# Optimization experiments

Hardware: AMD Instinct MI355X
Metric: run time of the kernel (lower is better)

Reference implementation:

```python
import jax, jax.numpy as jnp
import numpy as np

B, S, D, H, DK, F, K = 8, 1024, 512, 8, 64, 2048, 31
EPS = 1e-5


def _ln(x, g, b):
    m = jnp.mean(x, -1, keepdims=True)
    v = jnp.mean((x - m) ** 2, -1, keepdims=True)
    return (x - m) * jax.lax.rsqrt(v + EPS) * g + b


def _ff(x, w1, b1, w2, b2):
    return jnp.maximum(x @ w1 + b1, 0.0) @ w2 + b2


def setup_inputs() -> dict:
    key = jax.random.key(0)
    ks = jax.random.split(key, 16)
    w = lambda k, shape: jax.random.normal(k, shape, dtype=jnp.float32) * 0.02
    inp = {"x": jax.random.normal(ks[0], (B, S, D), dtype=jnp.float32)}
    for name in ["norm1", "norm2", "norm3", "norm4", "conv_ln"]:
        inp[name + "_g"] = jnp.ones((D,), jnp.float32)
        inp[name + "_b"] = jnp.zeros((D,), jnp.float32)
    # feed-forward 1 and 2
    inp["ff1_w1"] = w(ks[1], (D, F)); inp["ff1_b1"] = jnp.zeros((F,), jnp.float32)
    inp["ff1_w2"] = w(ks[2], (F, D)); inp["ff1_b2"] = jnp.zeros((D,), jnp.float32)
    inp["ff2_w1"] = w(ks[3], (D, F)); inp["ff2_b1"] = jnp.zeros((F,), jnp.float32)
    inp["ff2_w2"] = w(ks[4], (F, D)); inp["ff2_b2"] = jnp.zeros((D,), jnp.float32)
    # attention projections ([in, out] layout)
    inp["wq"] = w(ks[5], (D, D)); inp["bq"] = jnp.zeros((D,), jnp.float32)
    inp["wk"] = w(ks[6], (D, D)); inp["bk"] = jnp.zeros((D,), jnp.float32)
    inp["wv"] = w(ks[7], (D, D)); inp["bv"] = jnp.zeros((D,), jnp.float32)
    inp["wo"] = w(ks[8], (D, D)); inp["bo"] = jnp.zeros((D,), jnp.float32)
    # convolution module
    inp["pw1_w"] = w(ks[9], (D, 2 * D)); inp["pw1_b"] = jnp.zeros((2 * D,), jnp.float32)
    inp["dw_w"] = w(ks[10], (D, 1, K)); inp["dw_b"] = jnp.zeros((D,), jnp.float32)
    inp["bn_g"] = jnp.ones((D,), jnp.float32); inp["bn_b"] = jnp.zeros((D,), jnp.float32)
    inp["bn_mean"] = jnp.zeros((D,), jnp.float32); inp["bn_var"] = jnp.ones((D,), jnp.float32)
    inp["pw2_w"] = w(ks[11], (D, D)); inp["pw2_b"] = jnp.zeros((D,), jnp.float32)
    return inp


def _forward(x, norm1_g, norm1_b, norm2_g, norm2_b, norm3_g, norm3_b, norm4_g, norm4_b,
             ff1_w1, ff1_b1, ff1_w2, ff1_b2, wq, bq, wk, bk, wv, bv, wo, bo,
             conv_ln_g, conv_ln_b, pw1_w, pw1_b, dw_w, dw_b,
             bn_g, bn_b, bn_mean, bn_var, pw2_w, pw2_b,
             ff2_w1, ff2_b1, ff2_w2, ff2_b2):
    b, s, _ = x.shape
    # half-step FF1
    x = x + 0.5 * _ff(_ln(x, norm1_g, norm1_b), ff1_w1, ff1_b1, ff1_w2, ff1_b2)
    # multi-head self-attention (pre-norm)
    h = _ln(x, norm2_g, norm2_b)
    q = (h @ wq + bq).reshape(b, s, H, DK)
    k = (h @ wk + bk).reshape(b, s, H, DK)
    v = (h @ wv + bv).reshape(b, s, H, DK)
    scores = jnp.einsum("bqhd,bkhd->bhqk", q, k) / jnp.sqrt(jnp.asarray(DK, x.dtype))
    attn = jax.nn.softmax(scores, axis=-1)
    o = jnp.einsum("bhqk,bkhd->bqhd", attn, v).reshape(b, s, D)
    x = x + (o @ wo + bo)
    # convolution module (pre-norm)
    h = _ln(x, norm3_g, norm3_b)
    h = _ln(h, conv_ln_g, conv_ln_b)
    h = h @ pw1_w + pw1_b                                 # [B,S,2D] pointwise conv1
    h = h[..., :D] * jax.nn.sigmoid(h[..., D:])           # GLU over channels
    h = h.transpose(0, 2, 1)                              # [B,D,S]
    h = jax.lax.conv_general_dilated(
        h, dw_w, window_strides=(1,), padding=((K // 2, K // 2),),
        feature_group_count=D, dimension_numbers=("NCH", "OIH", "NCH")) + dw_b[:, None]
    h = (h - bn_mean[:, None]) * jax.lax.rsqrt(bn_var + EPS)[:, None] * bn_g[:, None] + bn_b[:, None]
    h = h * jax.nn.sigmoid(h)                             # SiLU
    h = jnp.einsum("bcl,co->bol", h, pw2_w) + pw2_b[:, None]
    x = x + h.transpose(0, 2, 1)
    # half-step FF2
    x = x + 0.5 * _ff(_ln(x, norm4_g, norm4_b), ff2_w1, ff2_b1, ff2_w2, ff2_b2)
    return x


def reference(x, norm1_g, norm1_b, norm2_g, norm2_b, norm3_g, norm3_b, norm4_g, norm4_b,
              conv_ln_g, conv_ln_b, ff1_w1, ff1_b1, ff1_w2, ff1_b2,
              ff2_w1, ff2_b1, ff2_w2, ff2_b2, wq, bq, wk, bk, wv, bv, wo, bo,
              pw1_w, pw1_b, dw_w, dw_b, bn_g, bn_b, bn_mean, bn_var, pw2_w, pw2_b):
    return _forward(x, norm1_g, norm1_b, norm2_g, norm2_b, norm3_g, norm3_b, norm4_g, norm4_b,
                    ff1_w1, ff1_b1, ff1_w2, ff1_b2, wq, bq, wk, bk, wv, bv, wo, bo,
                    conv_ln_g, conv_ln_b, pw1_w, pw1_b, dw_w, dw_b,
                    bn_g, bn_b, bn_mean, bn_var, pw2_w, pw2_b,
                    ff2_w1, ff2_b1, ff2_w2, ff2_b2)
```

## Files before the change

### kernel.cpp

```cpp
#include <hip/hip_runtime.h>
#include <math.h>

#define TOK    8192
#define DMODEL 512
#define FDIM   2048
#define NH     8
#define DKH    64
#define SEQ    1024
#define BATCH  8
#define KCONV  31
#define LN_EPS 1e-5f

typedef __attribute__((ext_vector_type(8))) short bf16x8;
typedef __attribute__((ext_vector_type(4))) float f32x4;
typedef unsigned short ushort_t;

__device__ __forceinline__ float sigf(float x) { return 1.0f / (1.0f + __expf(-x)); }

__device__ __forceinline__ unsigned short f2bf(float f) {
  unsigned u = __float_as_uint(f);
  u = u + 0x7fffu + ((u >> 16) & 1u);
  return (unsigned short)(u >> 16);
}
__device__ __forceinline__ unsigned pk2(float a, float b) {
  return (unsigned)f2bf(a) | ((unsigned)f2bf(b) << 16);
}
__device__ __forceinline__ float bf2f(ushort_t u) {
  return __uint_as_float((unsigned)u << 16);
}

struct WJob { const float* src; ushort_t* dst; int K, N, t0; };
struct WJobs { WJob j[10]; };

__global__ __launch_bounds__(256) void wcast_all(WJobs jobs) {
  __shared__ float tile[32][33];
  const int t = blockIdx.x;
  int i = 0;
#pragma unroll
  for (int k = 1; k < 10; ++k) if (t >= jobs.j[k].t0) i = k;
  const WJob jb = jobs.j[i];
  const int local = t - jb.t0;
  const int ntx = jb.N >> 5;
  const int bx = (local % ntx) * 32, by = (local / ntx) * 32;
  const int tx = threadIdx.x, ty = threadIdx.y;
#pragma unroll
  for (int r = 0; r < 32; r += 8)
    tile[ty + r][tx] = jb.src[(size_t)(by + ty + r) * jb.N + bx + tx];
  __syncthreads();
#pragma unroll
  for (int r = 0; r < 32; r += 8)
    jb.dst[(size_t)(bx + ty + r) * jb.K + by + tx] = f2bf(tile[tx][ty + r]);
}

__global__ void misc_prep(const float* __restrict__ w, float* __restrict__ wT,
                          const float* __restrict__ bq, const float* __restrict__ bk,
                          const float* __restrict__ bv, float* __restrict__ bcat) {
  const int idx = blockIdx.x * 256 + threadIdx.x;
  if (idx < DMODEL * KCONV) {
    const int d = idx / KCONV, k = idx % KCONV;
    wT[k * DMODEL + d] = w[idx];
  } else if (idx < DMODEL * KCONV + 3 * DMODEL) {
    const int c = idx - DMODEL * KCONV;
    bcat[c] = (c < DMODEL) ? bq[c] : (c < 2 * DMODEL ? bk[c - DMODEL] : bv[c - 2 * DMODEL]);
  }
}

template <bool OBF>
__global__ __launch_bounds__(256) void ln_kernel(const float* __restrict__ in,
                                                 const float* __restrict__ g,
                                                 const float* __restrict__ b,
                                                 void* __restrict__ outp) {
  const int wave = threadIdx.x >> 6, lane = threadIdx.x & 63;
  const size_t row = (size_t)blockIdx.x * 4 + wave;
  const float* p = in + row * DMODEL + lane * 8;
  const float4 v0 = *(const float4*)p;
  const float4 v1 = *(const float4*)(p + 4);
  float s  = v0.x + v0.y + v0.z + v0.w + v1.x + v1.y + v1.z + v1.w;
  float ss = v0.x*v0.x + v0.y*v0.y + v0.z*v0.z + v0.w*v0.w
           + v1.x*v1.x + v1.y*v1.y + v1.z*v1.z + v1.w*v1.w;
#pragma unroll
  for (int m = 1; m < 64; m <<= 1) { s += __shfl_xor(s, m); ss += __shfl_xor(ss, m); }
  const float mean = s * (1.0f / DMODEL);
  const float var  = ss * (1.0f / DMODEL) - mean * mean;
  const float rstd = rsqrtf(var + LN_EPS);
  const float4 g0 = *(const float4*)(g + lane * 8);
  const float4 g1 = *(const float4*)(g + lane * 8 + 4);
  const float4 bb0 = *(const float4*)(b + lane * 8);
  const float4 bb1 = *(const float4*)(b + lane * 8 + 4);
  float o[8];
  o[0] = (v0.x - mean) * rstd * g0.x + bb0.x;
  o[1] = (v0.y - mean) * rstd * g0.y + bb0.y;
  o[2] = (v0.z - mean) * rstd * g0.z + bb0.z;
  o[3] = (v0.w - mean) * rstd * g0.w + bb0.w;
  o[4] = (v1.x - mean) * rstd * g1.x + bb1.x;
  o[5] = (v1.y - mean) * rstd * g1.y + bb1.y;
  o[6] = (v1.z - mean) * rstd * g1.z + bb1.z;
  o[7] = (v1.w - mean) * rstd * g1.w + bb1.w;
  if (OBF) {
    uint4 pkv;
    pkv.x = pk2(o[0], o[1]); pkv.y = pk2(o[2], o[3]);
    pkv.z = pk2(o[4], o[5]); pkv.w = pk2(o[6], o[7]);
    *(uint4*)((ushort_t*)outp + row * DMODEL + lane * 8) = pkv;
  } else {
    float4 a, c;
    a.x = o[0]; a.y = o[1]; a.z = o[2]; a.w = o[3];
    c.x = o[4]; c.y = o[5]; c.z = o[6]; c.w = o[7];
    float* q = (float*)outp + row * DMODEL + lane * 8;
    *(float4*)q = a;
    *(float4*)(q + 4) = c;
  }
}

__global__ __launch_bounds__(256) void ln2_kernel(const float* __restrict__ in,
                                                  const float* __restrict__ g1,
                                                  const float* __restrict__ b1,
                                                  const float* __restrict__ g2,
                                                  const float* __restrict__ b2,
                                                  ushort_t* __restrict__ outp) {
  const int wave = threadIdx.x >> 6, lane = threadIdx.x & 63;
  const size_t row = (size_t)blockIdx.x * 4 + wave;
  const float* p = in + row * DMODEL + lane * 8;
  float v[8];
  {
    const float4 v0 = *(const float4*)p;
    const float4 v1 = *(const float4*)(p + 4);
    v[0]=v0.x; v[1]=v0.y; v[2]=v0.z; v[3]=v0.w;
    v[4]=v1.x; v[5]=v1.y; v[6]=v1.z; v[7]=v1.w;
  }
  float s = 0.f, ss = 0.f;
#pragma unroll
  for (int e = 0; e < 8; ++e) { s += v[e]; ss += v[e]*v[e]; }
#pragma unroll
  for (int m = 1; m < 64; m <<= 1) { s += __shfl_xor(s, m); ss += __shfl_xor(ss, m); }
  float mean = s * (1.0f / DMODEL);
  float rstd = rsqrtf(ss * (1.0f / DMODEL) - mean * mean + LN_EPS);
  const float4 ga = *(const float4*)(g1 + lane * 8);
  const float4 gb = *(const float4*)(g1 + lane * 8 + 4);
  const float4 ba = *(const float4*)(b1 + lane * 8);
  const float4 bb = *(const float4*)(b1 + lane * 8 + 4);
  const float gg1[8] = {ga.x,ga.y,ga.z,ga.w,gb.x,gb.y,gb.z,gb.w};
  const float bb1[8] = {ba.x,ba.y,ba.z,ba.w,bb.x,bb.y,bb.z,bb.w};
#pragma unroll
  for (int e = 0; e < 8; ++e) v[e] = (v[e] - mean) * rstd * gg1[e] + bb1[e];
  s = 0.f; ss = 0.f;
#pragma unroll
  for (int e = 0; e < 8; ++e) { s += v[e]; ss += v[e]*v[e]; }
#pragma unroll
  for (int m = 1; m < 64; m <<= 1) { s += __shfl_xor(s, m); ss += __shfl_xor(ss, m); }
  mean = s * (1.0f / DMODEL);
  rstd = rsqrtf(ss * (1.0f / DMODEL) - mean * mean + LN_EPS);
  const float4 gc = *(const float4*)(g2 + lane * 8);
  const float4 gd = *(const float4*)(g2 + lane * 8 + 4);
  const float4 bc = *(const float4*)(b2 + lane * 8);
  const float4 bd = *(const float4*)(b2 + lane * 8 + 4);
  const float gg2[8] = {gc.x,gc.y,gc.z,gc.w,gd.x,gd.y,gd.z,gd.w};
  const float bb2[8] = {bc.x,bc.y,bc.z,bc.w,bd.x,bd.y,bd.z,bd.w};
  float o[8];
#pragma unroll
  for (int e = 0; e < 8; ++e) o[e] = (v[e] - mean) * rstd * gg2[e] + bb2[e];
  uint4 pkv;
  pkv.x = pk2(o[0], o[1]); pkv.y = pk2(o[2], o[3]);
  pkv.z = pk2(o[4], o[5]); pkv.w = pk2(o[6], o[7]);
  *(uint4*)(outp + row * DMODEL + lane * 8) = pkv;
}

template <int TN, int ACT, bool RES, bool OBF, bool QSC>
__global__ __launch_bounds__(256) void gemm_bf16(const ushort_t* __restrict__ A,
                                                 const ushort_t* __restrict__ Bt,
                                                 const float* __restrict__ bias,
                                                 const float* __restrict__ Rp,
                                                 float alpha,
                                                 void* __restrict__ Cout,
                                                 int M, int N, int K) {
  constexpr int NF = TN / 32;
  constexpr int NB = TN / 32;
  __shared__ ushort_t Al[128 * 64];
  __shared__ ushort_t Bl[TN * 64];
  const int t = threadIdx.x;
  const int lane = t & 63;
  const int wid = t >> 6;
  const int wr = wid >> 1, wc = wid & 1;
  const int m0 = blockIdx.y * 128, n0 = blockIdx.x * TN;

  f32x4 acc[4][NF];
#pragma unroll
  for (int m = 0; m < 4; ++m)
#pragma unroll
    for (int n = 0; n < NF; ++n) acc[m][n] = (f32x4){0.f, 0.f, 0.f, 0.f};

  const int srow = t >> 3;
  const int scol = (t & 7) * 8;
  const ushort_t* Ag = A + (size_t)(m0 + srow) * K + scol;
  const ushort_t* Bg = Bt + (size_t)(n0 + srow) * K + scol;

  for (int k0 = 0; k0 < K; k0 += 64) {
    __syncthreads();
#pragma unroll
    for (int i = 0; i < 4; ++i) {
      __builtin_amdgcn_global_load_lds(
          (const __attribute__((address_space(1))) unsigned*)(Ag + (size_t)i * 32 * K + k0),
          (__attribute__((address_space(3))) unsigned*)(Al + ((size_t)i * 256 + t) * 8),
          16, 0, 0);
    }
#pragma unroll
    for (int i = 0; i < NB; ++i) {
      __builtin_amdgcn_global_load_lds(
          (const __attribute__((address_space(1))) unsigned*)(Bg + (size_t)i * 32 * K + k0),
          (__attribute__((address_space(3))) unsigned*)(Bl + ((size_t)i * 256 + t) * 8),
          16, 0, 0);
    }
    __syncthreads();

#pragma unroll
    for (int ks = 0; ks < 2; ++ks) {
      const int kk = ks * 32 + (lane >> 4) * 8;
      bf16x8 af[4], bfv[NF];
#pragma unroll
      for (int m = 0; m < 4; ++m)
        af[m] = *(const bf16x8*)(Al + (wr * 64 + m * 16 + (lane & 15)) * 64 + kk);
#pragma unroll
      for (int n = 0; n < NF; ++n)
        bfv[n] = *(const bf16x8*)(Bl + (wc * (TN / 2) + n * 16 + (lane & 15)) * 64 + kk);
#pragma unroll
      for (int m = 0; m < 4; ++m)
#pragma unroll
        for (int n = 0; n < NF; ++n)
          acc[m][n] = __builtin_amdgcn_mfma_f32_16x16x32_bf16(af[m], bfv[n], acc[m][n], 0, 0, 0);
    }
  }

#pragma unroll
  for (int m = 0; m < 4; ++m) {
    const int row_b = m0 + wr * 64 + m * 16 + (lane >> 4) * 4;
#pragma unroll
    for (int n = 0; n < NF; ++n) {
      const int col = n0 + wc * (TN / 2) + n * 16 + (lane & 15);
      const float bv = bias[col];
#pragma unroll
      for (int j = 0; j < 4; ++j) {
        float v = acc[m][n][j] + bv;
        if (ACT == 1) v = fmaxf(v, 0.f);
        if (QSC) v *= (col < DMODEL ? 0.125f : 1.0f);
        const size_t idx = (size_t)(row_b + j) * N + col;
        if (RES) v = Rp[idx] + alpha * v;
        if (OBF) ((ushort_t*)Cout)[idx] = f2bf(v);
        else     ((float*)Cout)[idx] = v;
      }
    }
  }
}

__global__ __launch_bounds__(256) void vtrans(const ushort_t* __restrict__ QKV,
                                              ushort_t* __restrict__ Vt) {
  __shared__ ushort_t tl[64][72];
  const int st = blockIdx.x;
  const int bh = blockIdx.y;
  const int b = bh >> 3, h = bh & 7;
  const int t = threadIdx.x;
#pragma unroll
  for (int i = 0; i < 2; ++i) {
    const int chunk = i * 256 + t;
    const int sr = chunk >> 3, c8 = (chunk & 7) * 8;
    *(uint4*)&tl[sr][c8] =
        *(const uint4*)(QKV + ((size_t)(b * SEQ + st * 64 + sr) * (3 * DMODEL)) + 2 * DMODEL + h * DKH + c8);
  }
  __syncthreads();
#pragma unroll
  for (int i = 0; i < 2; ++i) {
    const int chunk = i * 256 + t;
    const int dr = chunk >> 3, c8 = (chunk & 7) * 8;
    ushort_t tmp[8];
#pragma unroll
    for (int e = 0; e < 8; ++e) tmp[e] = tl[c8 + e][dr];
    *(uint4*)(Vt + ((size_t)(bh * DKH + dr) * SEQ) + st * 64 + c8) = *(uint4*)tmp;
  }
}

__global__ __launch_bounds__(256) void attn_mfma(const ushort_t* __restrict__ QKV,
                                                 const ushort_t* __restrict__ Vt,
                                                 ushort_t* __restrict__ Om) {
  __shared__ ushort_t Ks[128 * 64];
  __shared__ ushort_t Vs[64 * 128];
  __shared__ ushort_t Ps[64 * 128];
  const int t = threadIdx.x;
  const int l = t & 63;
  const int w = t >> 6;
  const int qb = blockIdx.x, h = blockIdx.y, b = blockIdx.z;
  const size_t rowstr = 3 * DMODEL;
  const size_t baseQ = ((size_t)b * SEQ) * rowstr + (size_t)h * DKH;
  const size_t baseK = baseQ + DMODEL;
  const size_t baseV = (size_t)(b * NH + h) * DKH * SEQ;
  const size_t baseO = ((size_t)b * SEQ) * DMODEL + (size_t)h * DKH;

  bf16x8 qf[2];
  {
    const int qrow = qb * 64 + w * 16 + (l & 15);
    const ushort_t* qp = QKV + baseQ + (size_t)qrow * rowstr + ((l >> 4) * 8);
    qf[0] = *(const bf16x8*)(qp);
    qf[1] = *(const bf16x8*)(qp + 32);
  }

  float mrun[4], lrun[4];
  f32x4 o[4];
#pragma unroll
  for (int j = 0; j < 4; ++j) { mrun[j] = -1e30f; lrun[j] = 0.f; }
#pragma unroll
  for (int n = 0; n < 4; ++n) o[n] = (f32x4){0.f, 0.f, 0.f, 0.f};

  for (int kt = 0; kt < SEQ / 128; ++kt) {
    __syncthreads();
#pragma unroll
    for (int i = 0; i < 4; ++i) {
      const int chunk = i * 256 + t;
      {
        const int r = chunk >> 3, c8 = (chunk & 7) * 8;
        const uint4 kv = *(const uint4*)(QKV + baseK + (size_t)(kt * 128 + r) * rowstr + c8);
        *(uint4*)((char*)Ks + r * 128 + ((c8 * 2) ^ ((r & 7) << 4))) = kv;
      }
      {
        const int r = chunk >> 4, c8 = (chunk & 15) * 8;
        const uint4 vv = *(const uint4*)(Vt + baseV + (size_t)r * SEQ + kt * 128 + c8);
        *(uint4*)((char*)Vs + r * 256 + ((c8 * 2) ^ ((r & 15) << 4))) = vv;
      }
    }
    __syncthreads();

    f32x4 s[8];
#pragma unroll
    for (int n = 0; n < 8; ++n) s[n] = (f32x4){0.f, 0.f, 0.f, 0.f};
#pragma unroll
    for (int ks = 0; ks < 2; ++ks) {
      const int kk = ks * 64 + (l >> 4) * 16;
#pragma unroll
      for (int n = 0; n < 8; ++n) {
        const int krow = n * 16 + (l & 15);
        const bf16x8 kf = *(const bf16x8*)((char*)Ks + krow * 128 + (kk ^ ((krow & 7) << 4)));
        s[n] = __builtin_amdgcn_mfma_f32_16x16x32_bf16(qf[ks], kf, s[n], 0, 0, 0);
      }
    }

#pragma unroll
    for (int j = 0; j < 4; ++j) {
      float r0 = s[0][j];
#pragma unroll
      for (int n = 1; n < 8; ++n) r0 = fmaxf(r0, s[n][j]);
      r0 = fmaxf(r0, __shfl_xor(r0, 1));
      r0 = fmaxf(r0, __shfl_xor(r0, 2));
      r0 = fmaxf(r0, __shfl_xor(r0, 4));
      r0 = fmaxf(r0, __shfl_xor(r0, 8));
      const float mn = fmaxf(mrun[j], r0);
      const float cs = __expf(mrun[j] - mn);
      const int prow = w * 16 + (l >> 4) * 4 + j;
      const int pswz = (prow & 15) << 4;
      float psum = 0.f;
#pragma unroll
      for (int n = 0; n < 8; ++n) {
        const float p = __expf(s[n][j] - mn);
        psum += p;
        const int col2 = (n * 16 + (l & 15)) * 2;
        *(ushort_t*)((char*)Ps + prow * 256 + (col2 ^ pswz)) = f2bf(p);
      }
      psum += __shfl_xor(psum, 1);
      psum += __shfl_xor(psum, 2);
      psum += __shfl_xor(psum, 4);
      psum += __shfl_xor(psum, 8);
      lrun[j] = lrun[j] * cs + psum;
      mrun[j] = mn;
      o[0][j] *= cs; o[1][j] *= cs; o[2][j] *= cs; o[3][j] *= cs;
    }

#pragma unroll
    for (int ks = 0; ks < 4; ++ks) {
      const int kk = ks * 64 + (l >> 4) * 16;
      const int arow = w * 16 + (l & 15);
      const bf16x8 pf = *(const bf16x8*)((char*)Ps + arow * 256 + (kk ^ ((arow & 15) << 4)));
#pragma unroll
      for (int n = 0; n < 4; ++n) {
        const int vrow = n * 16 + (l & 15);
        const bf16x8 vf = *(const bf16x8*)((char*)Vs + vrow * 256 + (kk ^ ((vrow & 15) << 4)));
        o[n] = __builtin_amdgcn_mfma_f32_16x16x32_bf16(pf, vf, o[n], 0, 0, 0);
      }
    }
  }

  float inv[4];
#pragma unroll
  for (int j = 0; j < 4; ++j) inv[j] = 1.0f / lrun[j];
#pragma unroll
  for (int j = 0; j < 4; ++j) {
    const int prow = w * 16 + (l >> 4) * 4 + j;
    const int pswz = (prow & 15) << 4;
#pragma unroll
    for (int n = 0; n < 4; ++n) {
      const int col2 = (n * 16 + (l & 15)) * 2;
      *(ushort_t*)((char*)Ps + prow * 256 + (col2 ^ pswz)) = f2bf(o[n][j] * inv[j]);
    }
  }
  __syncthreads();
#pragma unroll
  for (int i = 0; i < 2; ++i) {
    const int chunk = i * 256 + t;
    const int qr = chunk >> 3, c8 = (chunk & 7) * 8;
    const uint4 ov = *(const uint4*)((char*)Ps + qr * 256 + ((c8 * 2) ^ ((qr & 15) << 4)));
    *(uint4*)(Om + baseO + (size_t)(qb * 64 + qr) * DMODEL + c8) = ov;
  }
}

__global__ __launch_bounds__(256) void glu_kernel(const ushort_t* __restrict__ in,
                                                  ushort_t* __restrict__ out) {
  const size_t gid = (size_t)blockIdx.x * 256 + threadIdx.x;
  const size_t row = gid >> 7;
  const int c = (int)(gid & 127) * 4;
  const ushort_t* p = in + row * (2 * DMODEL);
  ushort_t a[4], g[4];
  *(uint2*)a = *(const uint2*)(p + c);
  *(uint2*)g = *(const uint2*)(p + DMODEL + c);
  uint2 o;
  o.x = pk2(bf2f(a[0]) * sigf(bf2f(g[0])), bf2f(a[1]) * sigf(bf2f(g[1])));
  o.y = pk2(bf2f(a[2]) * sigf(bf2f(g[2])), bf2f(a[3]) * sigf(bf2f(g[3])));
  *(uint2*)&out[row * DMODEL + c] = o;
}

__global__ __launch_bounds__(256) void dwconv_bn_silu(const ushort_t* __restrict__ in,
                                                      const float* __restrict__ wT,
                                                      const float* __restrict__ dwb,
                                                      const float* __restrict__ bng,
                                                      const float* __restrict__ bnb,
                                                      const float* __restrict__ bnm,
                                                      const float* __restrict__ bnv,
                                                      ushort_t* __restrict__ out) {
  const size_t gid = (size_t)blockIdx.x * 256 + threadIdx.x;
  const int dc = (int)(gid & 127) * 4;
  const int s = (int)((gid >> 7) & (SEQ - 1));
  const int b = (int)(gid >> 17);
  const ushort_t* bp = in + (size_t)b * SEQ * DMODEL;
  float ax = 0.f, ay = 0.f, az = 0.f, aw = 0.f;
#pragma unroll
  for (int k = 0; k < KCONV; ++k) {
    const int ssi = s + k - (KCONV / 2);
    if (ssi < 0 || ssi >= SEQ) continue;
    ushort_t xv[4];
    *(uint2*)xv = *(const uint2*)(bp + (size_t)ssi * DMODEL + dc);
    const float4 w = *(const float4*)(wT + k * DMODEL + dc);
    ax = fmaf(bf2f(xv[0]), w.x, ax); ay = fmaf(bf2f(xv[1]), w.y, ay);
    az = fmaf(bf2f(xv[2]), w.z, az); aw = fmaf(bf2f(xv[3]), w.w, aw);
  }
  const float4 bi = *(const float4*)(dwb + dc);
  const float4 mm = *(const float4*)(bnm + dc);
  const float4 vv = *(const float4*)(bnv + dc);
  const float4 gg = *(const float4*)(bng + dc);
  const float4 b2 = *(const float4*)(bnb + dc);
  float v0 = ax + bi.x, v1 = ay + bi.y, v2 = az + bi.z, v3 = aw + bi.w;
  v0 = (v0 - mm.x) * rsqrtf(vv.x + LN_EPS) * gg.x + b2.x;
  v1 = (v1 - mm.y) * rsqrtf(vv.y + LN_EPS) * gg.y + b2.y;
  v2 = (v2 - mm.z) * rsqrtf(vv.z + LN_EPS) * gg.z + b2.z;
  v3 = (v3 - mm.w) * rsqrtf(vv.w + LN_EPS) * gg.w + b2.w;
  v0 = v0 * sigf(v0); v1 = v1 * sigf(v1); v2 = v2 * sigf(v2); v3 = v3 * sigf(v3);
  uint2 o;
  o.x = pk2(v0, v1); o.y = pk2(v2, v3);
  *(uint2*)&out[(((size_t)b * SEQ + s) * DMODEL) + dc] = o;
}

extern "C" void kernel_launch(void* const* d_in, const int* in_sizes, int n_in,
                              void* d_out, int out_size, void* d_ws, size_t ws_size,
                              hipStream_t stream) {
  const float* x    = (const float*)d_in[0];
  const float* n1g  = (const float*)d_in[1];
  const float* n1b  = (const float*)d_in[2];
  const float* n2g  = (const float*)d_in[3];
  const float* n2b  = (const float*)d_in[4];
  const float* n3g  = (const float*)d_in[5];
  const float* n3b  = (const float*)d_in[6];
  const float* n4g  = (const float*)d_in[7];
  const float* n4b  = (const float*)d_in[8];
  const float* clg  = (const float*)d_in[9];
  const float* clb  = (const float*)d_in[10];
  const float* f1w1 = (const float*)d_in[11];
  const float* f1b1 = (const float*)d_in[12];
  const float* f1w2 = (const float*)d_in[13];
  const float* f1b2 = (const float*)d_in[14];
  const float* f2w1 = (const float*)d_in[15];
  const float* f2b1 = (const float*)d_in[16];
  const float* f2w2 = (const float*)d_in[17];
  const float* f2b2 = (const float*)d_in[18];
  const float* wq   = (const float*)d_in[19];
  const float* bq   = (const float*)d_in[20];
  const float* wk   = (const float*)d_in[21];
  const float* bk   = (const float*)d_in[22];
  const float* wv   = (const float*)d_in[23];
  const float* bv   = (const float*)d_in[24];
  const float* wo   = (const float*)d_in[25];
  const float* bo   = (const float*)d_in[26];
  const float* pw1w = (const float*)d_in[27];
  const float* pw1b = (const float*)d_in[28];
  const float* dww  = (const float*)d_in[29];
  const float* dwb  = (const float*)d_in[30];
  const float* bng  = (const float*)d_in[31];
  const float* bnb  = (const float*)d_in[32];
  const float* bnm  = (const float*)d_in[33];
  const float* bnv  = (const float*)d_in[34];
  const float* pw2w = (const float*)d_in[35];
  const float* pw2b = (const float*)d_in[36];

  char* wsb = (char*)d_ws;
  const size_t MB = 1ull << 20;
  ushort_t* Wbf    = (ushort_t*)(wsb + 0);
  ushort_t* f1w1T  = Wbf + 0;
  ushort_t* f1w2T  = Wbf + (1ull << 20);
  ushort_t* f2w1T  = Wbf + (2ull << 20);
  ushort_t* f2w2T  = Wbf + (3ull << 20);
  ushort_t* wqkvT  = Wbf + (4ull << 20);
  ushort_t* wkT    = wqkvT + (256ull << 10);
  ushort_t* wvT    = wqkvT + (512ull << 10);
  ushort_t* woT    = wqkvT + (768ull << 10);
  ushort_t* pw1T   = Wbf + (5ull << 20);
  ushort_t* pw2T   = Wbf + (5ull << 20) + (512ull << 10);
  float*    WTc    = (float*)(wsb + 12 * MB);
  float*    bcat   = (float*)(wsb + 12 * MB + 128 * 1024);
  ushort_t* Lbf    = (ushort_t*)(wsb + 13 * MB);
  ushort_t* Hbf    = (ushort_t*)(wsb + 21 * MB);
  ushort_t* P1bf   = Hbf;
  ushort_t* QKVb   = (ushort_t*)(wsb + 53 * MB);
  ushort_t* Vtb    = (ushort_t*)(wsb + 77 * MB);
  ushort_t* Gbf    = (ushort_t*)(wsb + 53 * MB);
  ushort_t* Obf    = (ushort_t*)(wsb + 85 * MB);
  ushort_t* Cbf    = Obf;
  float* out = (float*)d_out;

  const dim3 blk(256);
  const dim3 blkT(32, 8);
  const dim3 gLN(TOK / 4);
  const dim3 gFFa(FDIM / 128, TOK / 128);
  const dim3 gFFb(DMODEL / 64, TOK / 128);
  const dim3 gQKV(3 * DMODEL / 128, TOK / 128);
  const dim3 gPW1(2 * DMODEL / 128, TOK / 128);
  const dim3 gAttn(SEQ / 64, NH, BATCH);
  const dim3 gVt(SEQ / 64, BATCH * NH);
  const dim3 gElem(TOK * 128 / 256);

  {
    WJobs jobs;
    const float* srcs[10] = {f1w1, f1w2, f2w1, f2w2, wq, wk, wv, wo, pw1w, pw2w};
    ushort_t* dsts[10] = {f1w1T, f1w2T, f2w1T, f2w2T, wqkvT, wkT, wvT, woT, pw1T, pw2T};
    const int Ks[10] = {512, 2048, 512, 2048, 512, 512, 512, 512, 512, 512};
    const int Ns[10] = {2048, 512, 2048, 512, 512, 512, 512, 512, 1024, 512};
    int t0 = 0;
    for (int i = 0; i < 10; ++i) {
      jobs.j[i].src = srcs[i]; jobs.j[i].dst = dsts[i];
      jobs.j[i].K = Ks[i]; jobs.j[i].N = Ns[i]; jobs.j[i].t0 = t0;
      t0 += (Ks[i] / 32) * (Ns[i] / 32);
    }
    wcast_all<<<t0, blkT, 0, stream>>>(jobs);
  }
  misc_prep<<<68, blk, 0, stream>>>(dww, WTc, bq, bk, bv, bcat);

  ln_kernel<true><<<gLN, blk, 0, stream>>>(x, n1g, n1b, Lbf);
  gemm_bf16<128, 1, false, true,  false><<<gFFa, blk, 0, stream>>>(Lbf, f1w1T, f1b1, nullptr, 0.f, Hbf, TOK, FDIM, DMODEL);
  gemm_bf16<64,  0, true,  false, false><<<gFFb, blk, 0, stream>>>(Hbf, f1w2T, f1b2, x, 0.5f, out, TOK, DMODEL, FDIM);

  ln_kernel<true><<<gLN, blk, 0, stream>>>(out, n2g, n2b, Lbf);
  gemm_bf16<128, 0, false, true,  true ><<<gQKV, blk, 0, stream>>>(Lbf, wqkvT, bcat, nullptr, 0.f, QKVb, TOK, 3 * DMODEL, DMODEL);
  vtrans<<<gVt, blk, 0, stream>>>(QKVb, Vtb);
  attn_mfma<<<gAttn, blk, 0, stream>>>(QKVb, Vtb, Obf);
  gemm_bf16<64,  0, true,  false, false><<<gFFb, blk, 0, stream>>>(Obf, woT, bo, out, 1.0f, out, TOK, DMODEL, DMODEL);

  ln2_kernel<<<gLN, blk, 0, stream>>>(out, n3g, n3b, clg, clb, Lbf);
  gemm_bf16<128, 0, false, true,  false><<<gPW1, blk, 0, stream>>>(Lbf, pw1T, pw1b, nullptr, 0.f, P1bf, TOK, 2 * DMODEL, DMODEL);
  glu_kernel<<<gElem, blk, 0, stream>>>(P1bf, Gbf);
  dwconv_bn_silu<<<gElem, blk, 0, stream>>>(Gbf, WTc, dwb, bng, bnb, bnm, bnv, Cbf);
  gemm_bf16<64,  0, true,  false, false><<<gFFb, blk, 0, stream>>>(Cbf, pw2T, pw2b, out, 1.0f, out, TOK, DMODEL, DMODEL);

  ln_kernel<true><<<gLN, blk, 0, stream>>>(out, n4g, n4b, Lbf);
  gemm_bf16<128, 1, false, true,  false><<<gFFa, blk, 0, stream>>>(Lbf, f2w1T, f2b1, nullptr, 0.f, Hbf, TOK, FDIM, DMODEL);
  gemm_bf16<64,  0, true,  false, false><<<gFFb, blk, 0, stream>>>(Hbf, f2w2T, f2b2, out, 0.5f, out, TOK, DMODEL, FDIM);
}
```

Baseline: 362.0 us.

## Fuse GLU into pointwise GEMM, swizzle blocks across XCDs, enlarge attention tiles

Three independent changes. First, GEMM block indices are remapped so consecutive tiles land on the same XCD, which should improve L2 reuse on MI355X. Second, the pw1 GEMM and the separate GLU kernel are merged into one kernel that computes the value and gate halves together and writes the gated bf16 output directly, removing the 2*D intermediate round trip and one launch. Third, attention now uses 512-thread blocks covering 128 query rows, so each K/V tile load is shared by twice as many queries, at the cost of larger LDS use and fewer blocks.

```diff
diff --git a/kernel.cpp b/kernel.cpp
--- a/kernel.cpp
+++ b/kernel.cpp
@@ -27,6 +27,15 @@
 }
 __device__ __forceinline__ float bf2f(ushort_t u) {
   return __uint_as_float((unsigned)u << 16);
+}
+
+__device__ __forceinline__ void xcd_swizzle(int gx, int* bx, int* by) {
+  const int nwg = gx * (int)gridDim.y;
+  const int cpx = nwg >> 3;
+  const int bid = (*by) * gx + (*bx);
+  const int wg = (bid & 7) * cpx + (bid >> 3);
+  *bx = wg % gx;
+  *by = wg / gx;
 }
 
 struct WJob { const float* src; ushort_t* dst; int K, N, t0; };
@@ -180,7 +189,9 @@
   const int lane = t & 63;
   const int wid = t >> 6;
   const int wr = wid >> 1, wc = wid & 1;
-  const int m0 = blockIdx.y * 128, n0 = blockIdx.x * TN;
+  int bx = blockIdx.x, by = blockIdx.y;
+  xcd_swizzle(gridDim.x, &bx, &by);
+  const int m0 = by * 128, n0 = bx * TN;
 
   f32x4 acc[4][NF];
 #pragma unroll
@@ -250,6 +261,98 @@
   }
 }
 
+__global__ __launch_bounds__(256) void gemm_glu(const ushort_t* __restrict__ A,
+                                                const ushort_t* __restrict__ Bt,
+                                                const float* __restrict__ bias,
+                                                ushort_t* __restrict__ Cout) {
+  __shared__ ushort_t Al[128 * 64];
+  __shared__ ushort_t Bl[128 * 64];
+  const int t = threadIdx.x;
+  const int lane = t & 63;
+  const int wid = t >> 6;
+  const int wr = wid >> 1, wc = wid & 1;
+  int bx = blockIdx.x, by = blockIdx.y;
+  xcd_swizzle(gridDim.x, &bx, &by);
+  const int m0 = by * 128, n0 = bx * 64;
+  const int K = DMODEL, N = DMODEL;
+
+  f32x4 aa[4][2], ag[4][2];
+#pragma unroll
+  for (int m = 0; m < 4; ++m)
+#pragma unroll
+    for (int n = 0; n < 2; ++n) {
+      aa[m][n] = (f32x4){0.f, 0.f, 0.f, 0.f};
+      ag[m][n] = (f32x4){0.f, 0.f, 0.f, 0.f};
+    }
+
+  const int srow = t >> 3;
+  const int scol = (t & 7) * 8;
+  const ushort_t* Ag_ = A + (size_t)(m0 + srow) * K + scol;
+  const ushort_t* Ba_ = Bt + (size_t)(n0 + srow) * K + scol;
+  const ushort_t* Bg_ = Bt + (size_t)(512 + n0 + srow) * K + scol;
+
+  for (int k0 = 0; k0 < K; k0 += 64) {
+    __syncthreads();
+#pragma unroll
+    for (int i = 0; i < 4; ++i) {
+      __builtin_amdgcn_global_load_lds(
+          (const __attribute__((address_space(1))) unsigned*)(Ag_ + (size_t)i * 32 * K + k0),
+          (__attribute__((address_space(3))) unsigned*)(Al + ((size_t)i * 256 + t) * 8),
+          16, 0, 0);
+    }
+#pragma unroll
+    for (int i = 0; i < 2; ++i) {
+      __builtin_amdgcn_global_load_lds(
+          (const __attribute__((address_space(1))) unsigned*)(Ba_ + (size_t)i * 32 * K + k0),
+          (__attribute__((address_space(3))) unsigned*)(Bl + ((size_t)i * 256 + t) * 8),
+          16, 0, 0);
+      __builtin_amdgcn_global_load_lds(
+          (const __attribute__((address_space(1))) unsigned*)(Bg_ + (size_t)i * 32 * K + k0),
+          (__attribute__((address_space(3))) unsigned*)(Bl + 64 * 64 + ((size_t)i * 256 + t) * 8),
+          16, 0, 0);
+    }
+    __syncthreads();
+
+#pragma unroll
+    for (int ks = 0; ks < 2; ++ks) {
+      const int kk = ks * 32 + (lane >> 4) * 8;
+      bf16x8 af[4], bfa[2], bfg[2];
+#pragma unroll
+      for (int m = 0; m < 4; ++m)
+        af[m] = *(const bf16x8*)(Al + (wr * 64 + m * 16 + (lane & 15)) * 64 + kk);
+#pragma unroll
+      for (int n = 0; n < 2; ++n) {
+        bfa[n] = *(const bf16x8*)(Bl + (wc * 32 + n * 16 + (lane & 15)) * 64 + kk);
+        bfg[n] = *(const bf16x8*)(Bl + (64 + wc * 32 + n * 16 + (lane & 15)) * 64 + kk);
+      }
+#pragma unroll
+      for (int m = 0; m < 4; ++m)
+#pragma unroll
+        for (int n = 0; n < 2; ++n) {
+          aa[m][n] = __builtin_amdgcn_mfma_f32_16x16x32_bf16(af[m], bfa[n], aa[m][n], 0, 0, 0);
+          ag[m][n] = __builtin_amdgcn_mfma_f32_16x16x32_bf16(af[m], bfg[n], ag[m][n], 0, 0, 0);
+        }
+    }
+  }
+
+#pragma unroll
+  for (int m = 0; m < 4; ++m) {
+    const int row_b = m0 + wr * 64 + m * 16 + (lane >> 4) * 4;
+#pragma unroll
+    for (int n = 0; n < 2; ++n) {
+      const int col = n0 + wc * 32 + n * 16 + (lane & 15);
+      const float ba_v = bias[col];
+      const float bg_v = bias[col + DMODEL];
+#pragma unroll
+      for (int j = 0; j < 4; ++j) {
+        const float av = aa[m][n][j] + ba_v;
+        const float gv = ag[m][n][j] + bg_v;
+        Cout[(size_t)(row_b + j) * N + col] = f2bf(av * sigf(gv));
+      }
+    }
+  }
+}
+
 __global__ __launch_bounds__(256) void vtrans(const ushort_t* __restrict__ QKV,
                                               ushort_t* __restrict__ Vt) {
   __shared__ ushort_t tl[64][72];
@@ -276,12 +379,12 @@
   }
 }
 
-__global__ __launch_bounds__(256) void attn_mfma(const ushort_t* __restrict__ QKV,
+__global__ __launch_bounds__(512) void attn_mfma(const ushort_t* __restrict__ QKV,
                                                  const ushort_t* __restrict__ Vt,
                                                  ushort_t* __restrict__ Om) {
   __shared__ ushort_t Ks[128 * 64];
   __shared__ ushort_t Vs[64 * 128];
-  __shared__ ushort_t Ps[64 * 128];
+  __shared__ ushort_t Ps[128 * 128];
   const int t = threadIdx.x;
   const int l = t & 63;
   const int w = t >> 6;
@@ -294,7 +397,7 @@
 
   bf16x8 qf[2];
   {
-    const int qrow = qb * 64 + w * 16 + (l & 15);
+    const int qrow = qb * 128 + w * 16 + (l & 15);
     const ushort_t* qp = QKV + baseQ + (size_t)qrow * rowstr + ((l >> 4) * 8);
     qf[0] = *(const bf16x8*)(qp);
     qf[1] = *(const bf16x8*)(qp + 32);
@@ -310,8 +413,8 @@
   for (int kt = 0; kt < SEQ / 128; ++kt) {
     __syncthreads();
 #pragma unroll
-    for (int i = 0; i < 4; ++i) {
-      const int chunk = i * 256 + t;
+    for (int i = 0; i < 2; ++i) {
+      const int chunk = i * 512 + t;
       {
         const int r = chunk >> 3, c8 = (chunk & 7) * 8;
         const uint4 kv = *(const uint4*)(QKV + baseK + (size_t)(kt * 128 + r) * rowstr + c8);
@@ -399,26 +502,11 @@
   __syncthreads();
 #pragma unroll
   for (int i = 0; i < 2; ++i) {
-    const int chunk = i * 256 + t;
+    const int chunk = i * 512 + t;
     const int qr = chunk >> 3, c8 = (chunk & 7) * 8;
     const uint4 ov = *(const uint4*)((char*)Ps + qr * 256 + ((c8 * 2) ^ ((qr & 15) << 4)));
-    *(uint4*)(Om + baseO + (size_t)(qb * 64 + qr) * DMODEL + c8) = ov;
-  }
-}
-
-__global__ __launch_bounds__(256) void glu_kernel(const ushort_t* __restrict__ in,
-                                                  ushort_t* __restrict__ out) {
-  const size_t gid = (size_t)blockIdx.x * 256 + threadIdx.x;
-  const size_t row = gid >> 7;
-  const int c = (int)(gid & 127) * 4;
-  const ushort_t* p = in + row * (2 * DMODEL);
-  ushort_t a[4], g[4];
-  *(uint2*)a = *(const uint2*)(p + c);
-  *(uint2*)g = *(const uint2*)(p + DMODEL + c);
-  uint2 o;
-  o.x = pk2(bf2f(a[0]) * sigf(bf2f(g[0])), bf2f(a[1]) * sigf(bf2f(g[1])));
-  o.y = pk2(bf2f(a[2]) * sigf(bf2f(g[2])), bf2f(a[3]) * sigf(bf2f(g[3])));
-  *(uint2*)&out[row * DMODEL + c] = o;
+    *(uint4*)(Om + baseO + (size_t)(qb * 128 + qr) * DMODEL + c8) = ov;
+  }
 }
 
 __global__ __launch_bounds__(256) void dwconv_bn_silu(const ushort_t* __restrict__ in,
@@ -519,7 +607,6 @@
   float*    bcat   = (float*)(wsb + 12 * MB + 128 * 1024);
   ushort_t* Lbf    = (ushort_t*)(wsb + 13 * MB);
   ushort_t* Hbf    = (ushort_t*)(wsb + 21 * MB);
-  ushort_t* P1bf   = Hbf;
   ushort_t* QKVb   = (ushort_t*)(wsb + 53 * MB);
   ushort_t* Vtb    = (ushort_t*)(wsb + 77 * MB);
   ushort_t* Gbf    = (ushort_t*)(wsb + 53 * MB);
@@ -528,13 +615,14 @@
   float* out = (float*)d_out;
 
   const dim3 blk(256);
+  const dim3 blk512(512);
   const dim3 blkT(32, 8);
   const dim3 gLN(TOK / 4);
   const dim3 gFFa(FDIM / 128, TOK / 128);
   const dim3 gFFb(DMODEL / 64, TOK / 128);
   const dim3 gQKV(3 * DMODEL / 128, TOK / 128);
-  const dim3 gPW1(2 * DMODEL / 128, TOK / 128);
-  const dim3 gAttn(SEQ / 64, NH, BATCH);
+  const dim3 gGLU(DMODEL / 64, TOK / 128);
+  const dim3 gAttn(SEQ / 128, NH, BATCH);
   const dim3 gVt(SEQ / 64, BATCH * NH);
   const dim3 gElem(TOK * 128 / 256);
 
@@ -561,12 +649,11 @@
   ln_kernel<true><<<gLN, blk, 0, stream>>>(out, n2g, n2b, Lbf);
   gemm_bf16<128, 0, false, true,  true ><<<gQKV, blk, 0, stream>>>(Lbf, wqkvT, bcat, nullptr, 0.f, QKVb, TOK, 3 * DMODEL, DMODEL);
   vtrans<<<gVt, blk, 0, stream>>>(QKVb, Vtb);
-  attn_mfma<<<gAttn, blk, 0, stream>>>(QKVb, Vtb, Obf);
+  attn_mfma<<<gAttn, blk512, 0, stream>>>(QKVb, Vtb, Obf);
   gemm_bf16<64,  0, true,  false, false><<<gFFb, blk, 0, stream>>>(Obf, woT, bo, out, 1.0f, out, TOK, DMODEL, DMODEL);
 
   ln2_kernel<<<gLN, blk, 0, stream>>>(out, n3g, n3b, clg, clb, Lbf);
-  gemm_bf16<128, 0, false, true,  false><<<gPW1, blk, 0, stream>>>(Lbf, pw1T, pw1b, nullptr, 0.f, P1bf, TOK, 2 * DMODEL, DMODEL);
-  glu_kernel<<<gElem, blk, 0, stream>>>(P1bf, Gbf);
+  gemm_glu<<<gGLU, blk, 0, stream>>>(Lbf, pw1T, pw1b, Gbf);
   dwconv_bn_silu<<<gElem, blk, 0, stream>>>(Gbf, WTc, dwb, bng, bnb, bnm, bnv, Cbf);
   gemm_bf16<64,  0, true,  false, false><<<gFFb, blk, 0, stream>>>(Cbf, pw2T, pw2b, out, 1.0f, out, TOK, DMODEL, DMODEL);
 
```

After: 352.2 us. 1.03x faster.
